# Kernel optimization log

Hardware: AMD Instinct MI355X
Metric: run time of the kernel (lower is better)

## Reference

```python
import jax, jax.numpy as jnp
import numpy as np

# Static diagonal offsets of the SparseDIA matrix (eqx static field).
OFFSETS = (-128, -64, -8, -1, 0, 1, 8, 64, 128)
N = 8192   # matrix dimension (diags.shape[1])
M = 4096   # number of dense columns in `other`


def setup_inputs() -> dict:
    key = jax.random.key(0)
    k1, k2 = jax.random.split(key)
    diags = jax.random.normal(k1, (len(OFFSETS), N), dtype=jnp.float32)
    other = jax.random.normal(k2, (N, M), dtype=jnp.float32)
    return {"diags": diags, "other": other}


def reference(diags, other):
    """SparseDIA._matmul_dense(left_matmul=True): out = A_dia @ other.

    For each static offset k, rows [top:bottom] of the output accumulate
    diag[start:end] (the valid part of the stored diagonal) times the
    matching rows of `other`. Offsets are Python ints, so all slices are
    static and jit-compatible.
    """
    n = other.shape[0]
    out = jnp.zeros_like(other)
    for k, offset in enumerate(OFFSETS):
        start = max(0, offset)
        end = min(n, n + offset)
        top = max(0, -offset)
        bottom = top + (end - start)
        out = out.at[top:bottom, :].add(
            diags[k, start:end, None] * other[start:end, :]
        )
    return out
```

## Files before the change

kernel.cpp:

```cpp
#include <hip/hip_runtime.h>


#define DIA_N 8192
#define DIA_M 4096
#define M4 (DIA_M / 4)

__global__ __launch_bounds__(256) void sparse_dia_kernel(
    const float* __restrict__ diags,
    const float* __restrict__ other,
    float* __restrict__ out)
{
    constexpr int OFF[9] = {-128, -64, -8, -1, 0, 1, 8, 64, 128};

    const int r  = blockIdx.y;
    const int c4 = blockIdx.x * blockDim.x + threadIdx.x;

    const float4* __restrict__ o4 = (const float4*)other;
    float4* __restrict__ out4     = (float4*)out;

    float4 acc = make_float4(0.f, 0.f, 0.f, 0.f);

    if (r >= 128 && r < DIA_N - 128) {
#pragma unroll
        for (int k = 0; k < 9; ++k) {
            const int q = r + OFF[k];
            const float d = diags[k * DIA_N + q];
            const float4 v = o4[q * M4 + c4];
            acc.x += d * v.x;
            acc.y += d * v.y;
            acc.z += d * v.z;
            acc.w += d * v.w;
        }
    } else {
#pragma unroll
        for (int k = 0; k < 9; ++k) {
            const int q = r + OFF[k];
            if (q >= 0 && q < DIA_N) {
                const float d = diags[k * DIA_N + q];
                const float4 v = o4[q * M4 + c4];
                acc.x += d * v.x;
                acc.y += d * v.y;
                acc.z += d * v.z;
                acc.w += d * v.w;
            }
        }
    }

    out4[r * M4 + c4] = acc;
}

extern "C" void kernel_launch(void* const* d_in, const int* in_sizes, int n_in,
                              void* d_out, int out_size, void* d_ws, size_t ws_size,
                              hipStream_t stream) {
    const float* diags = (const float*)d_in[0];
    const float* other = (const float*)d_in[1];
    float* out         = (float*)d_out;

    dim3 block(256, 1, 1);
    dim3 grid(M4 / 256, DIA_N, 1);
    sparse_dia_kernel<<<grid, block, 0, stream>>>(diags, other, out);
}
```

Before: 269.9 us.

## Register-tile 16 output rows per thread to reuse near-diagonal loads

Each thread now computes 16 consecutive output rows, so the five near-diagonal offsets (-8..8) share one load of each row of `other` across accumulators instead of reloading it per diagonal. The far offsets (±64, ±128) still load their rows separately. Output uses nontemporal stores and launch bounds request 4 blocks per SM. This raises register pressure (16 float4 accumulators) and cuts the grid to 1/16 as many blocks, which may lower occupancy and latency hiding.

```diff
diff --git a/kernel.cpp b/kernel.cpp
--- a/kernel.cpp
+++ b/kernel.cpp
@@ -4,49 +4,72 @@
 #define DIA_N 8192
 #define DIA_M 4096
 #define M4 (DIA_M / 4)
+#define TR 16
 
-__global__ __launch_bounds__(256) void sparse_dia_kernel(
+typedef float f4 __attribute__((ext_vector_type(4)));
+
+__global__ __launch_bounds__(256, 4) void sparse_dia_kernel(
     const float* __restrict__ diags,
     const float* __restrict__ other,
     float* __restrict__ out)
 {
-    constexpr int OFF[9] = {-128, -64, -8, -1, 0, 1, 8, 64, 128};
+    const int r0 = blockIdx.y * TR;
+    const int c4 = blockIdx.x * 256 + threadIdx.x;
 
-    const int r  = blockIdx.y;
-    const int c4 = blockIdx.x * blockDim.x + threadIdx.x;
+    const f4* __restrict__ o4 = (const f4*)other;
+    f4* __restrict__ out4     = (f4*)out;
 
-    const float4* __restrict__ o4 = (const float4*)other;
-    float4* __restrict__ out4     = (float4*)out;
+    f4 acc[TR];
+#pragma unroll
+    for (int i = 0; i < TR; ++i) acc[i] = (f4){0.f, 0.f, 0.f, 0.f};
 
-    float4 acc = make_float4(0.f, 0.f, 0.f, 0.f);
+    if (r0 >= 128 && r0 + TR + 128 <= DIA_N) {
 
-    if (r >= 128 && r < DIA_N - 128) {
+        constexpr int FOFF[4] = {-128, -64, 64, 128};
+        constexpr int FK[4]   = {0, 1, 7, 8};
+#pragma unroll
+        for (int f = 0; f < 4; ++f) {
+            const int off = FOFF[f];
+            const int k   = FK[f];
+#pragma unroll
+            for (int i = 0; i < TR; ++i) {
+                const int q   = r0 + i + off;
+                const float d = diags[k * DIA_N + q];
+                const f4 v    = o4[q * M4 + c4];
+                acc[i] += d * v;
+            }
+        }
+
+#pragma unroll
+        for (int j = -8; j < TR + 8; ++j) {
+            const int q = r0 + j;
+            const f4 v  = o4[q * M4 + c4];
+            if (j + 8 >= 0 && j + 8 < TR) acc[j + 8] += diags[2 * DIA_N + q] * v;
+            if (j + 1 >= 0 && j + 1 < TR) acc[j + 1] += diags[3 * DIA_N + q] * v;
+            if (j     >= 0 && j     < TR) acc[j    ] += diags[4 * DIA_N + q] * v;
+            if (j - 1 >= 0 && j - 1 < TR) acc[j - 1] += diags[5 * DIA_N + q] * v;
+            if (j - 8 >= 0 && j - 8 < TR) acc[j - 8] += diags[6 * DIA_N + q] * v;
+        }
+    } else {
+        constexpr int OFF[9] = {-128, -64, -8, -1, 0, 1, 8, 64, 128};
 #pragma unroll
         for (int k = 0; k < 9; ++k) {
-            const int q = r + OFF[k];
-            const float d = diags[k * DIA_N + q];
-            const float4 v = o4[q * M4 + c4];
-            acc.x += d * v.x;
-            acc.y += d * v.y;
-            acc.z += d * v.z;
-            acc.w += d * v.w;
-        }
-    } else {
 #pragma unroll
-        for (int k = 0; k < 9; ++k) {
-            const int q = r + OFF[k];
-            if (q >= 0 && q < DIA_N) {
-                const float d = diags[k * DIA_N + q];
-                const float4 v = o4[q * M4 + c4];
-                acc.x += d * v.x;
-                acc.y += d * v.y;
-                acc.z += d * v.z;
-                acc.w += d * v.w;
+            for (int i = 0; i < TR; ++i) {
+                const int q = r0 + i + OFF[k];
+                if (q >= 0 && q < DIA_N) {
+                    const float d = diags[k * DIA_N + q];
+                    const f4 v    = o4[q * M4 + c4];
+                    acc[i] += d * v;
+                }
             }
         }
     }
 
-    out4[r * M4 + c4] = acc;
+#pragma unroll
+    for (int i = 0; i < TR; ++i) {
+        __builtin_nontemporal_store(acc[i], &out4[(r0 + i) * M4 + c4]);
+    }
 }
 
 extern "C" void kernel_launch(void* const* d_in, const int* in_sizes, int n_in,
@@ -57,6 +80,6 @@
     float* out         = (float*)d_out;
 
     dim3 block(256, 1, 1);
-    dim3 grid(M4 / 256, DIA_N, 1);
+    dim3 grid(M4 / 256, DIA_N / TR, 1);
     sparse_dia_kernel<<<grid, block, 0, stream>>>(diags, other, out);
 }
```

Result: slower. 285.2 us (+5.7%).

## Tile rows with LDS halo window and async global-to-LDS loads

Applied to the files above, without the earlier changes.

Replaces the one-output-row-per-block scheme with blocks that cover 256 rows by 32 columns. Each block stages a 512-row halo window of `other` into LDS using global_load_lds, and stages the diagonals into LDS, so the nine shifted reads come from shared memory instead of nine separate global/L2 reads per output. The cost is halo overfetch (512 rows loaded for 256 outputs) plus about 66KB of LDS per block, which limits occupancy. Each block also has only narrow 128-byte row segments, and the window is loaded once with no overlap between loading and compute.

```diff
diff --git a/kernel.cpp b/kernel.cpp
--- a/kernel.cpp
+++ b/kernel.cpp
@@ -3,7 +3,17 @@
 
 #define DIA_N 8192
 #define DIA_M 4096
-#define M4 (DIA_M / 4)
+#define M4   (DIA_M / 4)
+#define CB   8
+#define BR   256
+#define HALO 128
+#define WIN  (BR + 2*HALO)
+#define TR   8
+
+typedef float f4 __attribute__((ext_vector_type(4)));
+
+typedef __attribute__((address_space(3))) unsigned int       lds_uint;
+typedef const __attribute__((address_space(1))) unsigned int glb_uint;
 
 __global__ __launch_bounds__(256) void sparse_dia_kernel(
     const float* __restrict__ diags,
@@ -12,41 +22,58 @@
 {
     constexpr int OFF[9] = {-128, -64, -8, -1, 0, 1, 8, 64, 128};
 
-    const int r  = blockIdx.y;
-    const int c4 = blockIdx.x * blockDim.x + threadIdx.x;
+    __shared__ f4    olds[WIN][CB];
+    __shared__ float dlds[9 * BR];
 
-    const float4* __restrict__ o4 = (const float4*)other;
-    float4* __restrict__ out4     = (float4*)out;
+    const int tid  = threadIdx.x;
+    const int r0   = blockIdx.y * BR;
+    const int cb4  = blockIdx.x * CB;
 
-    float4 acc = make_float4(0.f, 0.f, 0.f, 0.f);
+#pragma unroll
+    for (int f = tid; f < 9 * BR; f += 256) {
+        const int k = f >> 8;
+        const int i = f & (BR - 1);
+        const int q = r0 + i + OFF[k];
+        dlds[f] = (q >= 0 && q < DIA_N) ? diags[k * DIA_N + q] : 0.f;
+    }
 
-    if (r >= 128 && r < DIA_N - 128) {
+    {
+        const int wave = tid >> 6;
+        const int lane = tid & 63;
+        const int lrow = lane >> 3;
+        const int lcol = lane & 7;
 #pragma unroll
-        for (int k = 0; k < 9; ++k) {
-            const int q = r + OFF[k];
-            const float d = diags[k * DIA_N + q];
-            const float4 v = o4[q * M4 + c4];
-            acc.x += d * v.x;
-            acc.y += d * v.y;
-            acc.z += d * v.z;
-            acc.w += d * v.w;
-        }
-    } else {
-#pragma unroll
-        for (int k = 0; k < 9; ++k) {
-            const int q = r + OFF[k];
-            if (q >= 0 && q < DIA_N) {
-                const float d = diags[k * DIA_N + q];
-                const float4 v = o4[q * M4 + c4];
-                acc.x += d * v.x;
-                acc.y += d * v.y;
-                acc.z += d * v.z;
-                acc.w += d * v.w;
-            }
+        for (int s = 0; s < 16; ++s) {
+            const int chunk = wave * 16 + s;
+            int q = r0 - HALO + chunk * 8 + lrow;
+            q = (q < 0) ? 0 : (q >= DIA_N ? DIA_N - 1 : q);
+            const float* src = other + ((size_t)q * DIA_M + (size_t)(cb4 + lcol) * 4);
+            __builtin_amdgcn_global_load_lds(
+                (glb_uint*)src,
+                (lds_uint*)&olds[chunk * 8][0],
+                16, 0, 0);
         }
     }
 
-    out4[r * M4 + c4] = acc;
+    __syncthreads();
+
+    const int c  = tid & 7;
+    const int rt = tid >> 3;
+
+    const f4* __restrict__ ow = (const f4*)other; (void)ow;
+    f4* __restrict__ out4 = (f4*)out;
+
+#pragma unroll
+    for (int j = 0; j < TR; ++j) {
+        const int i  = rt * TR + j;
+        const int rl = HALO + i;
+        f4 a = (f4){0.f, 0.f, 0.f, 0.f};
+#pragma unroll
+        for (int k = 0; k < 9; ++k) {
+            a += dlds[k * BR + i] * olds[rl + OFF[k]][c];
+        }
+        out4[(size_t)(r0 + i) * M4 + cb4 + c] = a;
+    }
 }
 
 extern "C" void kernel_launch(void* const* d_in, const int* in_sizes, int n_in,
@@ -57,6 +84,6 @@
     float* out         = (float*)d_out;
 
     dim3 block(256, 1, 1);
-    dim3 grid(M4 / 256, DIA_N, 1);
+    dim3 grid(M4 / CB, DIA_N / BR, 1);
     sparse_dia_kernel<<<grid, block, 0, stream>>>(diags, other, out);
 }
```

Measured after the change: 260.8 us. -3.4%, faster.
